# Optimization experiments

Measured on AMD Instinct MI355X. Metric: run time of the kernel, lower is better.

## Reference

```python
import jax, jax.numpy as jnp
import numpy as np

B, CHAR_LEN, LSTM, VOCAB, NATTN = 4096, 64, 400, 73, 10

def _lstm_cell(x, h, c, W_ih, W_hh, b):
    # gates: [B, 4*LSTM] in (i, f, g, o) order, matching torch.nn.LSTMCell
    g = x @ W_ih.T + h @ W_hh.T + b
    i, f, gg, o = jnp.split(g, 4, axis=1)
    i = jax.nn.sigmoid(i); f = jax.nn.sigmoid(f)
    gg = jnp.tanh(gg); o = jax.nn.sigmoid(o)
    c_new = f * c + i * gg
    h_new = o * jnp.tanh(c_new)
    return h_new, c_new

def setup_inputs() -> dict:
    key = jax.random.key(0)
    ks = jax.random.split(key, 24)
    d = {}
    d['inputs'] = jax.random.normal(ks[0], (B, 3), jnp.float32)
    for n, k in zip(['h1','c1','h2','c2','h3','c3'], ks[1:7]):
        d[n] = jax.random.normal(k, (B, LSTM), jnp.float32) * 0.1
    d['kappa'] = jax.random.uniform(ks[7], (B, NATTN), jnp.float32) * 5.0
    d['w_prev'] = jax.random.uniform(ks[8], (B, VOCAB), jnp.float32)
    d['attention_values'] = jax.random.uniform(ks[9], (B, CHAR_LEN, VOCAB), jnp.float32)
    d['attention_lengths'] = jax.random.randint(ks[10], (B,), 1, CHAR_LEN + 1, jnp.int32)
    s = 0.05
    in1 = VOCAB + 3              # lstm1 input: [w, inputs]
    in23 = 3 + LSTM + VOCAB      # lstm2/3 input: [inputs, h, w]
    attn_in = VOCAB + 3 + LSTM
    d['W_ih1'] = jax.random.normal(ks[11], (4 * LSTM, in1), jnp.float32) * s
    d['W_hh1'] = jax.random.normal(ks[12], (4 * LSTM, LSTM), jnp.float32) * s
    d['b1'] = jax.random.normal(ks[13], (4 * LSTM,), jnp.float32) * s
    d['W_attn'] = jax.random.normal(ks[14], (3 * NATTN, attn_in), jnp.float32) * s
    d['b_attn'] = jax.random.normal(ks[15], (3 * NATTN,), jnp.float32) * s
    d['W_ih2'] = jax.random.normal(ks[16], (4 * LSTM, in23), jnp.float32) * s
    d['W_hh2'] = jax.random.normal(ks[17], (4 * LSTM, LSTM), jnp.float32) * s
    d['b2'] = jax.random.normal(ks[18], (4 * LSTM,), jnp.float32) * s
    d['W_ih3'] = jax.random.normal(ks[19], (4 * LSTM, in23), jnp.float32) * s
    d['W_hh3'] = jax.random.normal(ks[20], (4 * LSTM, LSTM), jnp.float32) * s
    d['b3'] = jax.random.normal(ks[21], (4 * LSTM,), jnp.float32) * s
    return d

def reference(inputs, h1, c1, h2, c2, h3, c3, kappa, w_prev, attention_values,
              attention_lengths, W_ih1, W_hh1, b1, W_attn, b_attn,
              W_ih2, W_hh2, b2, W_ih3, W_hh3, b3):
    char_len = attention_values.shape[1]
    # --- LSTM 1 ---
    s1_in = jnp.concatenate([w_prev, inputs], axis=1)
    h1n, c1n = _lstm_cell(s1_in, h1, c1, W_ih1, W_hh1, b1)
    # --- Gaussian-mixture location attention ---
    attn_in = jnp.concatenate([w_prev, inputs, h1n], axis=1)
    attn_params = jax.nn.softplus(attn_in @ W_attn.T + b_attn)
    alpha, beta, kap = jnp.split(attn_params, 3, axis=1)
    kap = kappa + kap / 25.0
    beta = jnp.maximum(beta, 0.01)
    u = jnp.arange(char_len, dtype=jnp.float32)[None, None, :]           # [1,1,C]
    phi = jnp.sum(alpha[:, :, None] *
                  jnp.exp(-jnp.square(kap[:, :, None] - u) / beta[:, :, None]),
                  axis=1)                                                 # [B,C]
    seq_mask = (jnp.arange(char_len)[None, :] < attention_lengths[:, None]).astype(jnp.float32)
    w = jnp.einsum('bc,bcv->bv', phi * seq_mask, attention_values)        # [B,V]
    # --- LSTM 2 & 3 ---
    s2_in = jnp.concatenate([inputs, h1n, w], axis=1)
    h2n, c2n = _lstm_cell(s2_in, h2, c2, W_ih2, W_hh2, b2)
    s3_in = jnp.concatenate([inputs, h2n, w], axis=1)
    h3n, c3n = _lstm_cell(s3_in, h3, c3, W_ih3, W_hh3, b3)
    return h3n
```

## Files before the change

kernel.cpp:

```cpp
#include <hip/hip_runtime.h>
#include <hip/hip_bf16.h>


#define B_SZ     4096
#define LSTM_N   400
#define NG       1600
#define NGP      1664
#define VOCAB    73
#define NATTN    10
#define CHARLEN  64
#define KP1      480
#define KP23     896

typedef _Float16 half8 __attribute__((ext_vector_type(8)));
typedef __attribute__((ext_vector_type(4))) float floatx4;

__device__ __forceinline__ void gload_lds16(const void* g, void* l) {
    __builtin_amdgcn_global_load_lds(
        (const __attribute__((address_space(1))) void*)g,
        (__attribute__((address_space(3))) void*)l, 16, 0, 0);
}

__device__ __forceinline__ int lds_slot(int r, int s) {
    return ((r >> 1) << 6) + (((((r & 1) << 2) | s) ^ ((r >> 1) & 7)) << 3);
}

__global__ __launch_bounds__(256) void pack_wall(const float* __restrict__ Wih1,
                                                 const float* __restrict__ Whh1,
                                                 const float* __restrict__ Wih2,
                                                 const float* __restrict__ Whh2,
                                                 const float* __restrict__ Wih3,
                                                 const float* __restrict__ Whh3,
                                                 const float* __restrict__ W_attn,
                                                 _Float16* __restrict__ W1,
                                                 _Float16* __restrict__ W2,
                                                 _Float16* __restrict__ W3,
                                                 _Float16* __restrict__ Wa)
{
    const int z = blockIdx.z;
    const int n = blockIdx.y;
    const int k = blockIdx.x * 256 + threadIdx.x;
    if (z == 3) {
        if (n >= 128 || k >= KP1) return;
        float v = (n < 30 && k < 476) ? W_attn[(size_t)n * 476 + k] : 0.f;
        Wa[(size_t)n * KP1 + k] = (_Float16)v;
        return;
    }
    const int u = n >> 2, g = n & 3;
    const int src = g * 400 + u;
    if (z == 0) {
        if (k >= KP1) return;
        float v = 0.f;
        if (u < 400) {
            if (k < 76)           v = Wih1[(size_t)src * 76 + k];
            else if (k < 476)     v = Whh1[(size_t)src * 400 + (k - 76)];
        }
        W1[(size_t)n * KP1 + k] = (_Float16)v;
    } else {
        if (k >= KP23) return;
        const float* Wih = (z == 1) ? Wih2 : Wih3;
        const float* Whh = (z == 1) ? Whh2 : Whh3;
        float v = 0.f;
        if (u < 400) {
            if (k < 476)          v = Wih[(size_t)src * 476 + k];
            else if (k < 876)     v = Whh[(size_t)src * 400 + (k - 476)];
        }
        ((z == 1) ? W2 : W3)[(size_t)n * KP23 + k] = (_Float16)v;
    }
}

__global__ __launch_bounds__(256) void pack_x(const float* __restrict__ w_prev,
                                              const float* __restrict__ inputs,
                                              const float* __restrict__ h1,
                                              const float* __restrict__ h2,
                                              const float* __restrict__ h3,
                                              _Float16* __restrict__ X1,
                                              _Float16* __restrict__ XA,
                                              _Float16* __restrict__ X2,
                                              _Float16* __restrict__ X3)
{
    const int b = blockIdx.y;
    const int k = blockIdx.x * 256 + threadIdx.x;
    if (k < KP1) {
        float v = 0.f;
        if (k < 73)        v = w_prev[(size_t)b * 73 + k];
        else if (k < 76)   v = inputs[(size_t)b * 3 + (k - 73)];
        else if (k < 476)  v = h1[(size_t)b * 400 + (k - 76)];
        X1[(size_t)b * KP1 + k] = (_Float16)v;
        if (k < 76 || k >= 476) XA[(size_t)b * KP1 + k] = (_Float16)v;
    }
    const int kk = k - KP1;
    if (kk >= 0 && kk < KP23) {
        if (kk >= 3 && kk < 476) return;
        float v2 = 0.f, v3 = 0.f;
        if (kk < 3) { v2 = inputs[(size_t)b * 3 + kk]; v3 = v2; }
        else if (kk >= 476 && kk < 876) {
            v2 = h2[(size_t)b * 400 + (kk - 476)];
            v3 = h3[(size_t)b * 400 + (kk - 476)];
        }
        X2[(size_t)b * KP23 + kk] = (_Float16)v2;
        X3[(size_t)b * KP23 + kk] = (_Float16)v3;
    }
}

__global__ __launch_bounds__(256) void gemm_fused(const _Float16* __restrict__ Wm,
                                                  const _Float16* __restrict__ X,
                                                  const float* __restrict__ bias,
                                                  const float* __restrict__ c_in,
                                                  _Float16* __restrict__ d1, int ld1,
                                                  _Float16* __restrict__ d2, int ld2,
                                                  float* __restrict__ fout, int Kp)
{
    __shared__ _Float16 As[128 * 32];
    __shared__ _Float16 Bs[128 * 32];

    const int t    = threadIdx.x;
    const int w    = t >> 6;
    const int lane = t & 63;
    const int quad = lane >> 4;
    const int l16  = lane & 15;
    const int m0   = blockIdx.y * 128;
    const int n0   = blockIdx.x * 128;
    const int wm   = (w >> 1) * 64;
    const int wn   = (w & 1) * 64;
    const int pr   = lane >> 3;
    const int sw8  = (lane & 7) ^ pr;
    const int rowo = (pr << 1) + (sw8 >> 2);
    const int ko   = (sw8 & 3) << 3;

    floatx4 acc[4][4] = {};

    for (int k0 = 0; k0 < Kp; k0 += 32) {
        __syncthreads();
#pragma unroll
        for (int j = 0; j < 2; j++) {
            const int cr = (j * 4 + w) * 16;
            gload_lds16(Wm + (size_t)(m0 + cr + rowo) * Kp + k0 + ko, As + cr * 32);
            gload_lds16(X  + (size_t)(n0 + cr + rowo) * Kp + k0 + ko, Bs + cr * 32);
        }
        asm volatile("s_waitcnt vmcnt(0)" ::: "memory");
        __syncthreads();

        half8 af[4], bf[4];
#pragma unroll
        for (int i = 0; i < 4; i++) {
            af[i] = *(const half8*)(As + lds_slot(wm + i * 16 + l16, quad));
            bf[i] = *(const half8*)(Bs + lds_slot(wn + i * 16 + l16, quad));
        }
#pragma unroll
        for (int mt = 0; mt < 4; mt++)
#pragma unroll
            for (int nt = 0; nt < 4; nt++)
                acc[mt][nt] = __builtin_amdgcn_mfma_f32_16x16x32_f16(
                    af[mt], bf[nt], acc[mt][nt], 0, 0, 0);
    }

#pragma unroll
    for (int mt = 0; mt < 4; mt++) {
        const int u = ((m0 + wm + mt * 16) >> 2) + quad;
        if (u >= LSTM_N) continue;
        const float bi = bias[u];
        const float bff = bias[400 + u];
        const float bg = bias[800 + u];
        const float bo = bias[1200 + u];
#pragma unroll
        for (int nt = 0; nt < 4; nt++) {
            const int b = n0 + wn + nt * 16 + l16;
            float gi = acc[mt][nt][0] + bi;
            float gf = acc[mt][nt][1] + bff;
            float gg = acc[mt][nt][2] + bg;
            float go = acc[mt][nt][3] + bo;
            float si = 1.f / (1.f + expf(-gi));
            float sf = 1.f / (1.f + expf(-gf));
            float so = 1.f / (1.f + expf(-go));
            float cn = sf * c_in[(size_t)b * LSTM_N + u] + si * tanhf(gg);
            float h  = so * tanhf(cn);
            if (fout) {
                fout[(size_t)b * LSTM_N + u] = h;
            } else {
                _Float16 hh = (_Float16)h;
                d1[(size_t)b * ld1 + u] = hh;
                if (d2) d2[(size_t)b * ld2 + u] = hh;
            }
        }
    }
}

__global__ __launch_bounds__(256) void gemm_plain(const _Float16* __restrict__ A,
                                                  const _Float16* __restrict__ Bw,
                                                  const float* __restrict__ bias,
                                                  float* __restrict__ C, int Kp,
                                                  int ldC, int Nvalid)
{
    __shared__ _Float16 As[128 * 32];
    __shared__ _Float16 Bs[128 * 32];

    const int t    = threadIdx.x;
    const int w    = t >> 6;
    const int lane = t & 63;
    const int quad = lane >> 4;
    const int l16  = lane & 15;
    const int m0   = blockIdx.y * 128;
    const int n0   = blockIdx.x * 128;
    const int wm   = (w >> 1) * 64;
    const int wn   = (w & 1) * 64;
    const int pr   = lane >> 3;
    const int sw8  = (lane & 7) ^ pr;
    const int rowo = (pr << 1) + (sw8 >> 2);
    const int ko   = (sw8 & 3) << 3;

    floatx4 acc[4][4] = {};

    for (int k0 = 0; k0 < Kp; k0 += 32) {
        __syncthreads();
#pragma unroll
        for (int j = 0; j < 2; j++) {
            const int cr = (j * 4 + w) * 16;
            gload_lds16(A  + (size_t)(m0 + cr + rowo) * Kp + k0 + ko, As + cr * 32);
            gload_lds16(Bw + (size_t)(n0 + cr + rowo) * Kp + k0 + ko, Bs + cr * 32);
        }
        asm volatile("s_waitcnt vmcnt(0)" ::: "memory");
        __syncthreads();

        half8 af[4], bf[4];
#pragma unroll
        for (int i = 0; i < 4; i++) {
            af[i] = *(const half8*)(As + lds_slot(wm + i * 16 + l16, quad));
            bf[i] = *(const half8*)(Bs + lds_slot(wn + i * 16 + l16, quad));
        }
#pragma unroll
        for (int mt = 0; mt < 4; mt++)
#pragma unroll
            for (int nt = 0; nt < 4; nt++)
                acc[mt][nt] = __builtin_amdgcn_mfma_f32_16x16x32_f16(
                    af[mt], bf[nt], acc[mt][nt], 0, 0, 0);
    }

#pragma unroll
    for (int nt = 0; nt < 4; nt++) {
        const int n = n0 + wn + nt * 16 + l16;
        if (n >= Nvalid) continue;
        const float bv = bias[n];
#pragma unroll
        for (int mt = 0; mt < 4; mt++) {
            const int mbase = m0 + wm + mt * 16 + quad * 4;
#pragma unroll
            for (int r = 0; r < 4; r++)
                C[(size_t)(mbase + r) * ldC + n] = acc[mt][nt][r] + bv;
        }
    }
}

__global__ __launch_bounds__(256) void attn_phi(const float* __restrict__ AP,
                                                const float* __restrict__ kappa,
                                                const float* __restrict__ AV,
                                                const int* __restrict__ alen,
                                                _Float16* __restrict__ X2,
                                                _Float16* __restrict__ X3)
{
    __shared__ float prm[4][32];
    __shared__ float phi_s[4][CHARLEN];

    const int t = threadIdx.x;
    const int wave = t >> 6;
    const int lane = t & 63;
    const int b = blockIdx.x * 4 + wave;

    if (lane < 30) {
        float p  = AP[(size_t)b * 32 + lane];
        float sp = (p > 20.f) ? p : log1pf(expf(p));
        float v;
        if (lane < 10)      v = sp;
        else if (lane < 20) v = fmaxf(sp, 0.01f);
        else                v = kappa[(size_t)b * NATTN + (lane - 20)] + sp * (1.f / 25.f);
        prm[wave][lane] = v;
    }
    __syncthreads();

    const int len = alen[b];
    {
        int c = lane;
        float phi = 0.f;
#pragma unroll
        for (int j = 0; j < NATTN; j++) {
            float d = prm[wave][20 + j] - (float)c;
            phi += prm[wave][j] * expf(-d * d / prm[wave][10 + j]);
        }
        phi_s[wave][c] = (c < len) ? phi : 0.f;
    }
    __syncthreads();

    for (int v0 = 0; v0 < VOCAB; v0 += 64) {
        const int v = v0 + lane;
        if (v < VOCAB) {
            const float* avb = AV + (size_t)b * CHARLEN * VOCAB + v;
            float s = 0.f;
            for (int c = 0; c < len; c++)
                s += phi_s[wave][c] * avb[(size_t)c * VOCAB];
            _Float16 wv = (_Float16)s;
            X2[(size_t)b * KP23 + 403 + v] = wv;
            X3[(size_t)b * KP23 + 403 + v] = wv;
        }
    }
}

extern "C" void kernel_launch(void* const* d_in, const int* in_sizes, int n_in,
                              void* d_out, int out_size, void* d_ws, size_t ws_size,
                              hipStream_t stream)
{
    const float* inputs = (const float*)d_in[0];
    const float* h1     = (const float*)d_in[1];
    const float* c1     = (const float*)d_in[2];
    const float* h2     = (const float*)d_in[3];
    const float* c2     = (const float*)d_in[4];
    const float* h3     = (const float*)d_in[5];
    const float* c3     = (const float*)d_in[6];
    const float* kappa  = (const float*)d_in[7];
    const float* w_prev = (const float*)d_in[8];
    const float* AV     = (const float*)d_in[9];
    const int*   alen   = (const int*)d_in[10];
    const float* W_ih1  = (const float*)d_in[11];
    const float* W_hh1  = (const float*)d_in[12];
    const float* b1     = (const float*)d_in[13];
    const float* W_attn = (const float*)d_in[14];
    const float* b_attn = (const float*)d_in[15];
    const float* W_ih2  = (const float*)d_in[16];
    const float* W_hh2  = (const float*)d_in[17];
    const float* b2     = (const float*)d_in[18];
    const float* W_ih3  = (const float*)d_in[19];
    const float* W_hh3  = (const float*)d_in[20];
    const float* b3     = (const float*)d_in[21];
    float* out = (float*)d_out;

    char* p = (char*)d_ws;
    _Float16* X1 = (_Float16*)p; p += (size_t)B_SZ * KP1 * 2;
    _Float16* XA = (_Float16*)p; p += (size_t)B_SZ * KP1 * 2;
    _Float16* X2 = (_Float16*)p; p += (size_t)B_SZ * KP23 * 2;
    _Float16* X3 = (_Float16*)p; p += (size_t)B_SZ * KP23 * 2;
    _Float16* W1 = (_Float16*)p; p += (size_t)NGP * KP1 * 2;
    _Float16* W2 = (_Float16*)p; p += (size_t)NGP * KP23 * 2;
    _Float16* W3 = (_Float16*)p; p += (size_t)NGP * KP23 * 2;
    _Float16* Wa = (_Float16*)p; p += (size_t)128 * KP1 * 2;
    float* AP = (float*)p;

    pack_wall<<<dim3(4, NGP, 4), 256, 0, stream>>>(W_ih1, W_hh1, W_ih2, W_hh2,
                                                   W_ih3, W_hh3, W_attn,
                                                   W1, W2, W3, Wa);
    pack_x<<<dim3((KP1 + KP23 + 255) / 256, B_SZ), 256, 0, stream>>>(
        w_prev, inputs, h1, h2, h3, X1, XA, X2, X3);

    const dim3 fgrid(B_SZ / 128, NGP / 128);

    gemm_fused<<<fgrid, 256, 0, stream>>>(W1, X1, b1, c1,
                                          XA + 76, KP1, X2 + 3, KP23, nullptr, KP1);
    gemm_plain<<<dim3(1, B_SZ / 128), 256, 0, stream>>>(XA, Wa, b_attn, AP, KP1, 32, 30);
    attn_phi<<<B_SZ / 4, 256, 0, stream>>>(AP, kappa, AV, alen, X2, X3);
    gemm_fused<<<fgrid, 256, 0, stream>>>(W2, X2, b2, c2,
                                          X3 + 3, KP23, nullptr, 0, nullptr, KP23);
    gemm_fused<<<fgrid, 256, 0, stream>>>(W3, X3, b3, c3,
                                          nullptr, 0, nullptr, 0, out, KP23);
}
```

Measured before the change: 323.1 us.

## Retile LSTM GEMMs to 64x128 tiles with K=64 steps and drop gate padding

The fused LSTM GEMM moves from 128x128 tiles with a K step of 32 to 64x128 tiles with a K step of 64, using a new LDS swizzle. This lets the gate dimension be exactly 1600 rows instead of padded 1664, removing wasted MFMA work and bounds checks. The attention projection GEMM is transposed so that batch is the N dimension and weights occupy a 64-row tile, which cuts its padded compute. KP1 grows to 512 to fit the K=64 step, adding some zero-padded work, and the smaller M tile lowers A-operand reuse per block while doubling the block count.

```diff
diff --git a/kernel.cpp b/kernel.cpp
--- a/kernel.cpp
+++ b/kernel.cpp
@@ -5,11 +5,10 @@
 #define B_SZ     4096
 #define LSTM_N   400
 #define NG       1600
-#define NGP      1664
 #define VOCAB    73
 #define NATTN    10
 #define CHARLEN  64
-#define KP1      480
+#define KP1      512
 #define KP23     896
 
 typedef _Float16 half8 __attribute__((ext_vector_type(8)));
@@ -21,8 +20,8 @@
         (__attribute__((address_space(3))) void*)l, 16, 0, 0);
 }
 
-__device__ __forceinline__ int lds_slot(int r, int s) {
-    return ((r >> 1) << 6) + (((((r & 1) << 2) | s) ^ ((r >> 1) & 7)) << 3);
+__device__ __forceinline__ int lds_off(int r, int g) {
+    return (r << 6) + ((((g ^ r) & 7)) << 3);
 }
 
 __global__ __launch_bounds__(256) void pack_wall(const float* __restrict__ Wih1,
@@ -41,30 +40,27 @@
     const int n = blockIdx.y;
     const int k = blockIdx.x * 256 + threadIdx.x;
     if (z == 3) {
-        if (n >= 128 || k >= KP1) return;
+        if (n >= 64 || k >= KP1) return;
         float v = (n < 30 && k < 476) ? W_attn[(size_t)n * 476 + k] : 0.f;
         Wa[(size_t)n * KP1 + k] = (_Float16)v;
         return;
     }
+    if (n >= NG) return;
     const int u = n >> 2, g = n & 3;
     const int src = g * 400 + u;
     if (z == 0) {
         if (k >= KP1) return;
         float v = 0.f;
-        if (u < 400) {
-            if (k < 76)           v = Wih1[(size_t)src * 76 + k];
-            else if (k < 476)     v = Whh1[(size_t)src * 400 + (k - 76)];
-        }
+        if (k < 76)           v = Wih1[(size_t)src * 76 + k];
+        else if (k < 476)     v = Whh1[(size_t)src * 400 + (k - 76)];
         W1[(size_t)n * KP1 + k] = (_Float16)v;
     } else {
         if (k >= KP23) return;
         const float* Wih = (z == 1) ? Wih2 : Wih3;
         const float* Whh = (z == 1) ? Whh2 : Whh3;
         float v = 0.f;
-        if (u < 400) {
-            if (k < 476)          v = Wih[(size_t)src * 476 + k];
-            else if (k < 876)     v = Whh[(size_t)src * 400 + (k - 476)];
-        }
+        if (k < 476)          v = Wih[(size_t)src * 476 + k];
+        else if (k < 876)     v = Whh[(size_t)src * 400 + (k - 476)];
         ((z == 1) ? W2 : W3)[(size_t)n * KP23 + k] = (_Float16)v;
     }
 }
@@ -111,58 +107,68 @@
                                                   _Float16* __restrict__ d2, int ld2,
                                                   float* __restrict__ fout, int Kp)
 {
-    __shared__ _Float16 As[128 * 32];
-    __shared__ _Float16 Bs[128 * 32];
+    __shared__ _Float16 As[64 * 64];
+    __shared__ _Float16 Bs[128 * 64];
 
     const int t    = threadIdx.x;
     const int w    = t >> 6;
     const int lane = t & 63;
     const int quad = lane >> 4;
     const int l16  = lane & 15;
-    const int m0   = blockIdx.y * 128;
+    const int m0   = blockIdx.y * 64;
     const int n0   = blockIdx.x * 128;
-    const int wm   = (w >> 1) * 64;
+    const int wm   = (w >> 1) * 32;
     const int wn   = (w & 1) * 64;
-    const int pr   = lane >> 3;
-    const int sw8  = (lane & 7) ^ pr;
-    const int rowo = (pr << 1) + (sw8 >> 2);
-    const int ko   = (sw8 & 3) << 3;
-
-    floatx4 acc[4][4] = {};
-
-    for (int k0 = 0; k0 < Kp; k0 += 32) {
+    const int lr   = lane >> 3;
+    const int gq   = (lane & 7) ^ lr;
+
+    floatx4 acc[2][4] = {};
+
+    for (int k0 = 0; k0 < Kp; k0 += 64) {
         __syncthreads();
+        {
+            const int cr = w * 16;
+#pragma unroll
+            for (int s = 0; s < 2; s++)
+                gload_lds16(Wm + (size_t)(m0 + cr + s * 8 + lr) * Kp + k0 + gq * 8,
+                            As + (cr + s * 8) * 64);
+        }
 #pragma unroll
         for (int j = 0; j < 2; j++) {
             const int cr = (j * 4 + w) * 16;
-            gload_lds16(Wm + (size_t)(m0 + cr + rowo) * Kp + k0 + ko, As + cr * 32);
-            gload_lds16(X  + (size_t)(n0 + cr + rowo) * Kp + k0 + ko, Bs + cr * 32);
+#pragma unroll
+            for (int s = 0; s < 2; s++)
+                gload_lds16(X + (size_t)(n0 + cr + s * 8 + lr) * Kp + k0 + gq * 8,
+                            Bs + (cr + s * 8) * 64);
         }
         asm volatile("s_waitcnt vmcnt(0)" ::: "memory");
         __syncthreads();
 
-        half8 af[4], bf[4];
-#pragma unroll
-        for (int i = 0; i < 4; i++) {
-            af[i] = *(const half8*)(As + lds_slot(wm + i * 16 + l16, quad));
-            bf[i] = *(const half8*)(Bs + lds_slot(wn + i * 16 + l16, quad));
-        }
-#pragma unroll
-        for (int mt = 0; mt < 4; mt++)
-#pragma unroll
-            for (int nt = 0; nt < 4; nt++)
-                acc[mt][nt] = __builtin_amdgcn_mfma_f32_16x16x32_f16(
-                    af[mt], bf[nt], acc[mt][nt], 0, 0, 0);
-    }
-
-#pragma unroll
-    for (int mt = 0; mt < 4; mt++) {
+#pragma unroll
+        for (int h = 0; h < 2; h++) {
+            half8 af[2], bf[4];
+#pragma unroll
+            for (int i = 0; i < 2; i++)
+                af[i] = *(const half8*)(As + lds_off(wm + i * 16 + l16, h * 4 + quad));
+#pragma unroll
+            for (int i = 0; i < 4; i++)
+                bf[i] = *(const half8*)(Bs + lds_off(wn + i * 16 + l16, h * 4 + quad));
+#pragma unroll
+            for (int mt = 0; mt < 2; mt++)
+#pragma unroll
+                for (int nt = 0; nt < 4; nt++)
+                    acc[mt][nt] = __builtin_amdgcn_mfma_f32_16x16x32_f16(
+                        af[mt], bf[nt], acc[mt][nt], 0, 0, 0);
+        }
+    }
+
+#pragma unroll
+    for (int mt = 0; mt < 2; mt++) {
         const int u = ((m0 + wm + mt * 16) >> 2) + quad;
-        if (u >= LSTM_N) continue;
-        const float bi = bias[u];
+        const float bi  = bias[u];
         const float bff = bias[400 + u];
-        const float bg = bias[800 + u];
-        const float bo = bias[1200 + u];
+        const float bg  = bias[800 + u];
+        const float bo  = bias[1200 + u];
 #pragma unroll
         for (int nt = 0; nt < 4; nt++) {
             const int b = n0 + wn + nt * 16 + l16;
@@ -186,67 +192,77 @@
     }
 }
 
-__global__ __launch_bounds__(256) void gemm_plain(const _Float16* __restrict__ A,
-                                                  const _Float16* __restrict__ Bw,
+__global__ __launch_bounds__(256) void gemm_plain(const _Float16* __restrict__ Wa,
+                                                  const _Float16* __restrict__ XA,
                                                   const float* __restrict__ bias,
-                                                  float* __restrict__ C, int Kp,
-                                                  int ldC, int Nvalid)
-{
-    __shared__ _Float16 As[128 * 32];
-    __shared__ _Float16 Bs[128 * 32];
+                                                  float* __restrict__ C, int Kp)
+{
+    __shared__ _Float16 As[64 * 64];
+    __shared__ _Float16 Bs[128 * 64];
 
     const int t    = threadIdx.x;
     const int w    = t >> 6;
     const int lane = t & 63;
     const int quad = lane >> 4;
     const int l16  = lane & 15;
-    const int m0   = blockIdx.y * 128;
     const int n0   = blockIdx.x * 128;
-    const int wm   = (w >> 1) * 64;
+    const int wm   = (w >> 1) * 32;
     const int wn   = (w & 1) * 64;
-    const int pr   = lane >> 3;
-    const int sw8  = (lane & 7) ^ pr;
-    const int rowo = (pr << 1) + (sw8 >> 2);
-    const int ko   = (sw8 & 3) << 3;
-
-    floatx4 acc[4][4] = {};
-
-    for (int k0 = 0; k0 < Kp; k0 += 32) {
+    const int lr   = lane >> 3;
+    const int gq   = (lane & 7) ^ lr;
+
+    floatx4 acc[2][4] = {};
+
+    for (int k0 = 0; k0 < Kp; k0 += 64) {
         __syncthreads();
+        {
+            const int cr = w * 16;
+#pragma unroll
+            for (int s = 0; s < 2; s++)
+                gload_lds16(Wa + (size_t)(cr + s * 8 + lr) * Kp + k0 + gq * 8,
+                            As + (cr + s * 8) * 64);
+        }
 #pragma unroll
         for (int j = 0; j < 2; j++) {
             const int cr = (j * 4 + w) * 16;
-            gload_lds16(A  + (size_t)(m0 + cr + rowo) * Kp + k0 + ko, As + cr * 32);
-            gload_lds16(Bw + (size_t)(n0 + cr + rowo) * Kp + k0 + ko, Bs + cr * 32);
+#pragma unroll
+            for (int s = 0; s < 2; s++)
+                gload_lds16(XA + (size_t)(n0 + cr + s * 8 + lr) * Kp + k0 + gq * 8,
+                            Bs + (cr + s * 8) * 64);
         }
         asm volatile("s_waitcnt vmcnt(0)" ::: "memory");
         __syncthreads();
 
-        half8 af[4], bf[4];
-#pragma unroll
-        for (int i = 0; i < 4; i++) {
-            af[i] = *(const half8*)(As + lds_slot(wm + i * 16 + l16, quad));
-            bf[i] = *(const half8*)(Bs + lds_slot(wn + i * 16 + l16, quad));
-        }
-#pragma unroll
-        for (int mt = 0; mt < 4; mt++)
-#pragma unroll
-            for (int nt = 0; nt < 4; nt++)
-                acc[mt][nt] = __builtin_amdgcn_mfma_f32_16x16x32_f16(
-                    af[mt], bf[nt], acc[mt][nt], 0, 0, 0);
-    }
-
-#pragma unroll
-    for (int nt = 0; nt < 4; nt++) {
-        const int n = n0 + wn + nt * 16 + l16;
-        if (n >= Nvalid) continue;
-        const float bv = bias[n];
-#pragma unroll
-        for (int mt = 0; mt < 4; mt++) {
-            const int mbase = m0 + wm + mt * 16 + quad * 4;
-#pragma unroll
-            for (int r = 0; r < 4; r++)
-                C[(size_t)(mbase + r) * ldC + n] = acc[mt][nt][r] + bv;
+#pragma unroll
+        for (int h = 0; h < 2; h++) {
+            half8 af[2], bf[4];
+#pragma unroll
+            for (int i = 0; i < 2; i++)
+                af[i] = *(const half8*)(As + lds_off(wm + i * 16 + l16, h * 4 + quad));
+#pragma unroll
+            for (int i = 0; i < 4; i++)
+                bf[i] = *(const half8*)(Bs + lds_off(wn + i * 16 + l16, h * 4 + quad));
+#pragma unroll
+            for (int mt = 0; mt < 2; mt++)
+#pragma unroll
+                for (int nt = 0; nt < 4; nt++)
+                    acc[mt][nt] = __builtin_amdgcn_mfma_f32_16x16x32_f16(
+                        af[mt], bf[nt], acc[mt][nt], 0, 0, 0);
+        }
+    }
+
+#pragma unroll
+    for (int mt = 0; mt < 2; mt++) {
+#pragma unroll
+        for (int r = 0; r < 4; r++) {
+            const int m = wm + mt * 16 + quad * 4 + r;
+            if (m >= 30) continue;
+            const float bv = bias[m];
+#pragma unroll
+            for (int nt = 0; nt < 4; nt++) {
+                const int b = n0 + wn + nt * 16 + l16;
+                C[(size_t)b * 32 + m] = acc[mt][nt][r] + bv;
+            }
         }
     }
 }
@@ -337,23 +353,23 @@
     _Float16* XA = (_Float16*)p; p += (size_t)B_SZ * KP1 * 2;
     _Float16* X2 = (_Float16*)p; p += (size_t)B_SZ * KP23 * 2;
     _Float16* X3 = (_Float16*)p; p += (size_t)B_SZ * KP23 * 2;
-    _Float16* W1 = (_Float16*)p; p += (size_t)NGP * KP1 * 2;
-    _Float16* W2 = (_Float16*)p; p += (size_t)NGP * KP23 * 2;
-    _Float16* W3 = (_Float16*)p; p += (size_t)NGP * KP23 * 2;
-    _Float16* Wa = (_Float16*)p; p += (size_t)128 * KP1 * 2;
+    _Float16* W1 = (_Float16*)p; p += (size_t)NG * KP1 * 2;
+    _Float16* W2 = (_Float16*)p; p += (size_t)NG * KP23 * 2;
+    _Float16* W3 = (_Float16*)p; p += (size_t)NG * KP23 * 2;
+    _Float16* Wa = (_Float16*)p; p += (size_t)64 * KP1 * 2;
     float* AP = (float*)p;
 
-    pack_wall<<<dim3(4, NGP, 4), 256, 0, stream>>>(W_ih1, W_hh1, W_ih2, W_hh2,
-                                                   W_ih3, W_hh3, W_attn,
-                                                   W1, W2, W3, Wa);
+    pack_wall<<<dim3(4, NG, 4), 256, 0, stream>>>(W_ih1, W_hh1, W_ih2, W_hh2,
+                                                  W_ih3, W_hh3, W_attn,
+                                                  W1, W2, W3, Wa);
     pack_x<<<dim3((KP1 + KP23 + 255) / 256, B_SZ), 256, 0, stream>>>(
         w_prev, inputs, h1, h2, h3, X1, XA, X2, X3);
 
-    const dim3 fgrid(B_SZ / 128, NGP / 128);
+    const dim3 fgrid(B_SZ / 128, NG / 64);
 
     gemm_fused<<<fgrid, 256, 0, stream>>>(W1, X1, b1, c1,
                                           XA + 76, KP1, X2 + 3, KP23, nullptr, KP1);
-    gemm_plain<<<dim3(1, B_SZ / 128), 256, 0, stream>>>(XA, Wa, b_attn, AP, KP1, 32, 30);
+    gemm_plain<<<dim3(B_SZ / 128, 1), 256, 0, stream>>>(Wa, XA, b_attn, AP, KP1);
     attn_phi<<<B_SZ / 4, 256, 0, stream>>>(AP, kappa, AV, alen, X2, X3);
     gemm_fused<<<fgrid, 256, 0, stream>>>(W2, X2, b2, c2,
                                           X3 + 3, KP23, nullptr, 0, nullptr, KP23);
```

After: 297.4 us. 8.0% less time.
